# Kernel optimization log

Measured on AMD Instinct MI355X. Metric: run time of the kernel, lower is better.

Reference implementation:

```python
import jax, jax.numpy as jnp
import numpy as np

N_ENT = 50000
N_REL = 500
N_EDGE = 800000
D_IN = 100
D_OUT = 100
ALPHA = 0.2  # LeakyReLU negative slope


def setup_inputs() -> dict:
    key = jax.random.key(0)
    k0, k1, k2, k3, k4 = jax.random.split(key, 5)
    entity_embedding = jax.random.normal(k0, (N_ENT, D_IN), dtype=jnp.float32) * 0.1
    relation_embedding = jax.random.normal(k1, (N_REL, D_IN), dtype=jnp.float32) * 0.1
    W = jax.random.normal(k2, (D_IN, D_OUT), dtype=jnp.float32) * 0.1
    edge_index = jax.random.randint(k3, (2, N_EDGE), 0, N_ENT, dtype=jnp.int32)
    edge_type = jax.random.randint(k4, (N_EDGE,), 0, N_REL, dtype=jnp.int32)
    return {
        "entity_embedding": entity_embedding,
        "relation_embedding": relation_embedding,
        "W": W,
        "edge_index": edge_index,
        "edge_type": edge_type,
    }


def reference(entity_embedding, relation_embedding, W, edge_index, edge_type):
    N = entity_embedding.shape[0]
    # project input embeddings with shared W (in_features -> out_features)
    ent = entity_embedding @ W          # [N_ent, D]
    rel = relation_embedding @ W        # [N_rel, D]

    h = edge_index[0]                   # destination / head nodes [E]
    t = edge_index[1]                   # source / tail nodes      [E]

    # TransE edge score: ||h + r - t||_2 per edge
    diff = ent[h] + rel[edge_type] - ent[t]          # [E, D]
    score = jnp.sqrt(jnp.sum(diff * diff, axis=1))   # [E]
    e = jax.nn.leaky_relu(score, negative_slope=ALPHA)

    # scatter-softmax over edges grouped by head node
    seg_max = jax.ops.segment_max(e, h, num_segments=N)         # [N]
    seg_max = jnp.where(jnp.isfinite(seg_max), seg_max, 0.0)    # empty segments -> -inf
    ex = jnp.exp(e - seg_max[h])                                 # [E]
    denom = jax.ops.segment_sum(ex, h, num_segments=N)          # [N]
    att = ex / (denom[h] + 1e-16)                                # [E]

    # message: composition 'sub' of tail embedding and relation, weighted by attention
    msg = (ent[t] - rel[edge_type]) * att[:, None]               # [E, D]
    out = jax.ops.segment_sum(msg, h, num_segments=N)            # [N, D]

    # concat=True -> nonlinearity (ELU, standard GAT behavior)
    return jax.nn.elu(out)
```

## Files before the change

### kernel.cpp

```cpp
#include <hip/hip_runtime.h>
#include <math.h>

#define N_ENT  50000
#define N_REL  500
#define N_EDGE 800000
#define D      100
#define ALPHA  0.2f

#define SCAN_B 256
#define NBLK_SCAN ((N_ENT + SCAN_B - 1) / SCAN_B)

#define PROJ_TPB  256
#define PROJ_RPB  50
#define PROJ_RPT  25
#define WT_STRIDE 101

__global__ __launch_bounds__(PROJ_TPB) void proj_kernel(const float* __restrict__ X,
                                                        const float* __restrict__ W,
                                                        float* __restrict__ Y) {
    __shared__ float WT[D * WT_STRIDE];
    __shared__ float Xs[PROJ_RPB * D];
    int t = threadIdx.x;

    for (int i = t; i < D * D; i += PROJ_TPB) {
        int k = i / D, c = i % D;
        WT[c * WT_STRIDE + k] = W[i];
    }
    size_t xbase = (size_t)blockIdx.x * PROJ_RPB * D;
    for (int i = t; i < PROJ_RPB * D; i += PROJ_TPB)
        Xs[i] = X[xbase + i];
    __syncthreads();

    if (t < 200) {
        int c  = t % 100;
        int r0 = (t / 100) * PROJ_RPT;
        const float* wt = &WT[c * WT_STRIDE];
        for (int j = 0; j < PROJ_RPT; j += 5) {
            const float* x0 = &Xs[(r0 + j    ) * D];
            const float* x1 = &Xs[(r0 + j + 1) * D];
            const float* x2 = &Xs[(r0 + j + 2) * D];
            const float* x3 = &Xs[(r0 + j + 3) * D];
            const float* x4 = &Xs[(r0 + j + 4) * D];
            float a0 = 0.f, a1 = 0.f, a2 = 0.f, a3 = 0.f, a4 = 0.f;
            #pragma unroll
            for (int k = 0; k < D; ++k) {
                float w = wt[k];
                a0 = fmaf(x0[k], w, a0);
                a1 = fmaf(x1[k], w, a1);
                a2 = fmaf(x2[k], w, a2);
                a3 = fmaf(x3[k], w, a3);
                a4 = fmaf(x4[k], w, a4);
            }
            Y[xbase + (size_t)(r0 + j    ) * D + c] = a0;
            Y[xbase + (size_t)(r0 + j + 1) * D + c] = a1;
            Y[xbase + (size_t)(r0 + j + 2) * D + c] = a2;
            Y[xbase + (size_t)(r0 + j + 3) * D + c] = a3;
            Y[xbase + (size_t)(r0 + j + 4) * D + c] = a4;
        }
    }
}

__global__ void degree_kernel(const int* __restrict__ h_idx, int* __restrict__ deg) {
    int e = blockIdx.x * blockDim.x + threadIdx.x;
    if (e < N_EDGE) atomicAdd(&deg[h_idx[e]], 1);
}

__global__ void scan1_kernel(const int* __restrict__ deg, int* __restrict__ bsum) {
    __shared__ int s[SCAN_B];
    int i = blockIdx.x * SCAN_B + threadIdx.x;
    s[threadIdx.x] = (i < N_ENT) ? deg[i] : 0;
    __syncthreads();
    for (int off = SCAN_B / 2; off; off >>= 1) {
        if (threadIdx.x < off) s[threadIdx.x] += s[threadIdx.x + off];
        __syncthreads();
    }
    if (threadIdx.x == 0) bsum[blockIdx.x] = s[0];
}

__global__ void scan2_kernel(const int* __restrict__ bsum, int* __restrict__ boff) {
    __shared__ int s[SCAN_B];
    int tid = threadIdx.x;
    int v = (tid < NBLK_SCAN) ? bsum[tid] : 0;
    s[tid] = v;
    __syncthreads();
    for (int off = 1; off < SCAN_B; off <<= 1) {
        int x = (tid >= off) ? s[tid - off] : 0;
        __syncthreads();
        s[tid] += x;
        __syncthreads();
    }
    if (tid < NBLK_SCAN) boff[tid] = s[tid] - v;
}

__global__ void scan3_kernel(const int* __restrict__ deg, const int* __restrict__ boff,
                             int* __restrict__ rowptr, int* __restrict__ cursor) {
    __shared__ int s[SCAN_B];
    int tid = threadIdx.x;
    int i = blockIdx.x * SCAN_B + tid;
    int v = (i < N_ENT) ? deg[i] : 0;
    s[tid] = v;
    __syncthreads();
    for (int off = 1; off < SCAN_B; off <<= 1) {
        int x = (tid >= off) ? s[tid - off] : 0;
        __syncthreads();
        s[tid] += x;
        __syncthreads();
    }
    int excl = s[tid] - v + boff[blockIdx.x];
    if (i < N_ENT) { rowptr[i] = excl; cursor[i] = excl; }
    if (i == N_ENT - 1) rowptr[N_ENT] = excl + v;
}

__global__ void fill_kernel(const int* __restrict__ h_idx, const int* __restrict__ t_idx,
                            const int* __restrict__ etype, int* __restrict__ cursor,
                            int2* __restrict__ tr_sorted) {
    int e = blockIdx.x * blockDim.x + threadIdx.x;
    if (e >= N_EDGE) return;
    int h = h_idx[e];
    int pos = atomicAdd(&cursor[h], 1);
    tr_sorted[pos] = make_int2(t_idx[e], etype[e]);
}

__device__ __forceinline__ float edge_reduce32(const float4& eh, const float4& v) {
    float dx = eh.x + v.x, dy = eh.y + v.y, dz = eh.z + v.z, dw = eh.w + v.w;
    float s = dx * dx;
    s = fmaf(dy, dy, s);
    s = fmaf(dz, dz, s);
    s = fmaf(dw, dw, s);
    #pragma unroll
    for (int off = 16; off; off >>= 1) s += __shfl_xor(s, off, 32);
    return sqrtf(s);
}

__global__ __launch_bounds__(256) void fused_kernel(const float* __restrict__ ent,
                                                    const float* __restrict__ rel,
                                                    const int* __restrict__ rowptr,
                                                    const int2* __restrict__ tr_sorted,
                                                    float* __restrict__ out) {
    int head = blockIdx.x * 8 + (threadIdx.x >> 5);
    int lane = threadIdx.x & 31;
    if (head >= N_ENT) return;
    int beg = rowptr[head], end = rowptr[head + 1];

    float4 eh = make_float4(0.f, 0.f, 0.f, 0.f);
    if (lane < 25) eh = ((const float4*)(ent + (size_t)head * D))[lane];

    float  m   = -INFINITY;
    float  den = 0.f;
    float4 acc = make_float4(0.f, 0.f, 0.f, 0.f);

    int i = beg;
    for (; i + 1 < end; i += 2) {
        int2 e0 = tr_sorted[i];
        int2 e1 = tr_sorted[i + 1];
        float4 v0 = make_float4(0.f, 0.f, 0.f, 0.f);
        float4 v1 = make_float4(0.f, 0.f, 0.f, 0.f);
        if (lane < 25) {
            float4 et0 = ((const float4*)(ent + (size_t)e0.x * D))[lane];
            float4 er0 = ((const float4*)(rel + (size_t)e0.y * D))[lane];
            float4 et1 = ((const float4*)(ent + (size_t)e1.x * D))[lane];
            float4 er1 = ((const float4*)(rel + (size_t)e1.y * D))[lane];
            v0 = make_float4(er0.x - et0.x, er0.y - et0.y, er0.z - et0.z, er0.w - et0.w);
            v1 = make_float4(er1.x - et1.x, er1.y - et1.y, er1.z - et1.z, er1.w - et1.w);
        }
        float sc0 = edge_reduce32(eh, v0);
        float sc1 = edge_reduce32(eh, v1);

        float mn    = fmaxf(m, sc0);
        float scale = __expf(m - mn);
        float ex    = __expf(sc0 - mn);
        den   = den * scale + ex;
        acc.x = acc.x * scale - v0.x * ex;
        acc.y = acc.y * scale - v0.y * ex;
        acc.z = acc.z * scale - v0.z * ex;
        acc.w = acc.w * scale - v0.w * ex;
        m = mn;

        mn    = fmaxf(m, sc1);
        scale = __expf(m - mn);
        ex    = __expf(sc1 - mn);
        den   = den * scale + ex;
        acc.x = acc.x * scale - v1.x * ex;
        acc.y = acc.y * scale - v1.y * ex;
        acc.z = acc.z * scale - v1.z * ex;
        acc.w = acc.w * scale - v1.w * ex;
        m = mn;
    }
    if (i < end) {
        int2 e0 = tr_sorted[i];
        float4 v = make_float4(0.f, 0.f, 0.f, 0.f);
        if (lane < 25) {
            float4 et = ((const float4*)(ent + (size_t)e0.x * D))[lane];
            float4 er = ((const float4*)(rel + (size_t)e0.y * D))[lane];
            v = make_float4(er.x - et.x, er.y - et.y, er.z - et.z, er.w - et.w);
        }
        float sc = edge_reduce32(eh, v);
        float mn    = fmaxf(m, sc);
        float scale = __expf(m - mn);
        float ex    = __expf(sc - mn);
        den   = den * scale + ex;
        acc.x = acc.x * scale - v.x * ex;
        acc.y = acc.y * scale - v.y * ex;
        acc.z = acc.z * scale - v.z * ex;
        acc.w = acc.w * scale - v.w * ex;
        m = mn;
    }

    float inv = 1.f / (den + 1e-16f);
    float ox = acc.x * inv, oy = acc.y * inv, oz = acc.z * inv, ow = acc.w * inv;
    ox = ox > 0.f ? ox : expm1f(ox);
    oy = oy > 0.f ? oy : expm1f(oy);
    oz = oz > 0.f ? oz : expm1f(oz);
    ow = ow > 0.f ? ow : expm1f(ow);
    if (lane < 25)
        ((float4*)(out + (size_t)head * D))[lane] = make_float4(ox, oy, oz, ow);
}

extern "C" void kernel_launch(void* const* d_in, const int* in_sizes, int n_in,
                              void* d_out, int out_size, void* d_ws, size_t ws_size,
                              hipStream_t stream) {
    const float* entity_emb = (const float*)d_in[0];
    const float* rel_emb    = (const float*)d_in[1];
    const float* W          = (const float*)d_in[2];
    const int*   edge_index = (const int*)d_in[3];
    const int*   edge_type  = (const int*)d_in[4];
    float*       out        = (float*)d_out;

    const int* h_idx = edge_index;
    const int* t_idx = edge_index + N_EDGE;

    float* ent       = (float*)d_ws;
    float* rel       = ent + (size_t)N_ENT * D;
    int*   deg       = (int*)(rel + (size_t)N_REL * D);
    int*   rowptr    = deg + N_ENT;
    int*   cursor    = rowptr + (N_ENT + 1);
    int*   bsum      = cursor + N_ENT;
    int*   boff      = bsum + SCAN_B;
    int2*  tr_sorted = (int2*)(boff + SCAN_B);

    hipMemsetAsync(deg, 0, N_ENT * sizeof(int), stream);

    proj_kernel<<<N_ENT / PROJ_RPB, PROJ_TPB, 0, stream>>>(entity_emb, W, ent);
    proj_kernel<<<N_REL / PROJ_RPB, PROJ_TPB, 0, stream>>>(rel_emb, W, rel);

    degree_kernel<<<(N_EDGE + 255) / 256, 256, 0, stream>>>(h_idx, deg);
    scan1_kernel<<<NBLK_SCAN, SCAN_B, 0, stream>>>(deg, bsum);
    scan2_kernel<<<1, SCAN_B, 0, stream>>>(bsum, boff);
    scan3_kernel<<<NBLK_SCAN, SCAN_B, 0, stream>>>(deg, boff, rowptr, cursor);
    fill_kernel<<<(N_EDGE + 255) / 256, 256, 0, stream>>>(h_idx, t_idx, edge_type,
                                                          cursor, tr_sorted);

    fused_kernel<<<N_ENT / 8, 256, 0, stream>>>(ent, rel, rowptr, tr_sorted, out);
}
```

Baseline: 273.8 us.

## Merge projection launches, use single-block scan, unroll edge loop by four

The entity and relation projections now run in one launch, with the block index choosing the input. The three-kernel degree scan becomes a single 1024-thread block in which each thread handles 49 entries sequentially. The fused edge loop is unrolled by four so more gathers are in flight per warp. This removes three launches and their gaps and raises memory-level parallelism. The price is a serial single-block scan with strided, uncoalesced per-thread accesses, and higher register pressure in the fused kernel.

```diff
diff --git a/kernel.cpp b/kernel.cpp
--- a/kernel.cpp
+++ b/kernel.cpp
@@ -7,26 +7,33 @@
 #define D      100
 #define ALPHA  0.2f
 
-#define SCAN_B 256
-#define NBLK_SCAN ((N_ENT + SCAN_B - 1) / SCAN_B)
-
 #define PROJ_TPB  256
 #define PROJ_RPB  50
 #define PROJ_RPT  25
 #define WT_STRIDE 101
-
-__global__ __launch_bounds__(PROJ_TPB) void proj_kernel(const float* __restrict__ X,
+#define ENT_BLKS  (N_ENT / PROJ_RPB)
+#define REL_BLKS  (N_REL / PROJ_RPB)
+
+__global__ __launch_bounds__(PROJ_TPB) void proj_kernel(const float* __restrict__ Xe,
+                                                        const float* __restrict__ Xr,
                                                         const float* __restrict__ W,
-                                                        float* __restrict__ Y) {
+                                                        float* __restrict__ Ye,
+                                                        float* __restrict__ Yr) {
     __shared__ float WT[D * WT_STRIDE];
     __shared__ float Xs[PROJ_RPB * D];
     int t = threadIdx.x;
 
+    const float* X; float* Y; size_t xbase;
+    if (blockIdx.x < ENT_BLKS) {
+        X = Xe; Y = Ye; xbase = (size_t)blockIdx.x * PROJ_RPB * D;
+    } else {
+        X = Xr; Y = Yr; xbase = (size_t)(blockIdx.x - ENT_BLKS) * PROJ_RPB * D;
+    }
+
     for (int i = t; i < D * D; i += PROJ_TPB) {
         int k = i / D, c = i % D;
         WT[c * WT_STRIDE + k] = W[i];
     }
-    size_t xbase = (size_t)blockIdx.x * PROJ_RPB * D;
     for (int i = t; i < PROJ_RPB * D; i += PROJ_TPB)
         Xs[i] = X[xbase + i];
     __syncthreads();
@@ -65,50 +72,40 @@
     if (e < N_EDGE) atomicAdd(&deg[h_idx[e]], 1);
 }
 
-__global__ void scan1_kernel(const int* __restrict__ deg, int* __restrict__ bsum) {
-    __shared__ int s[SCAN_B];
-    int i = blockIdx.x * SCAN_B + threadIdx.x;
-    s[threadIdx.x] = (i < N_ENT) ? deg[i] : 0;
+#define SCAN_T   1024
+#define SCAN_EPT 49
+__global__ __launch_bounds__(SCAN_T) void scan_kernel(const int* __restrict__ deg,
+                                                      int* __restrict__ rowptr,
+                                                      int* __restrict__ cursor) {
+    __shared__ int s[SCAN_T];
+    int tid  = threadIdx.x;
+    int base = tid * SCAN_EPT;
+
+    int local = 0;
+    #pragma unroll 7
+    for (int j = 0; j < SCAN_EPT; ++j) {
+        int i = base + j;
+        if (i < N_ENT) local += deg[i];
+    }
+    s[tid] = local;
     __syncthreads();
-    for (int off = SCAN_B / 2; off; off >>= 1) {
-        if (threadIdx.x < off) s[threadIdx.x] += s[threadIdx.x + off];
-        __syncthreads();
-    }
-    if (threadIdx.x == 0) bsum[blockIdx.x] = s[0];
-}
-
-__global__ void scan2_kernel(const int* __restrict__ bsum, int* __restrict__ boff) {
-    __shared__ int s[SCAN_B];
-    int tid = threadIdx.x;
-    int v = (tid < NBLK_SCAN) ? bsum[tid] : 0;
-    s[tid] = v;
-    __syncthreads();
-    for (int off = 1; off < SCAN_B; off <<= 1) {
+    for (int off = 1; off < SCAN_T; off <<= 1) {
         int x = (tid >= off) ? s[tid - off] : 0;
         __syncthreads();
         s[tid] += x;
         __syncthreads();
     }
-    if (tid < NBLK_SCAN) boff[tid] = s[tid] - v;
-}
-
-__global__ void scan3_kernel(const int* __restrict__ deg, const int* __restrict__ boff,
-                             int* __restrict__ rowptr, int* __restrict__ cursor) {
-    __shared__ int s[SCAN_B];
-    int tid = threadIdx.x;
-    int i = blockIdx.x * SCAN_B + tid;
-    int v = (i < N_ENT) ? deg[i] : 0;
-    s[tid] = v;
-    __syncthreads();
-    for (int off = 1; off < SCAN_B; off <<= 1) {
-        int x = (tid >= off) ? s[tid - off] : 0;
-        __syncthreads();
-        s[tid] += x;
-        __syncthreads();
-    }
-    int excl = s[tid] - v + boff[blockIdx.x];
-    if (i < N_ENT) { rowptr[i] = excl; cursor[i] = excl; }
-    if (i == N_ENT - 1) rowptr[N_ENT] = excl + v;
+    int excl = s[tid] - local;
+    #pragma unroll 7
+    for (int j = 0; j < SCAN_EPT; ++j) {
+        int i = base + j;
+        if (i < N_ENT) {
+            rowptr[i] = excl;
+            cursor[i] = excl;
+            excl += deg[i];
+        }
+    }
+    if (tid == SCAN_T - 1) rowptr[N_ENT] = s[SCAN_T - 1];
 }
 
 __global__ void fill_kernel(const int* __restrict__ h_idx, const int* __restrict__ t_idx,
@@ -150,43 +147,38 @@
     float4 acc = make_float4(0.f, 0.f, 0.f, 0.f);
 
     int i = beg;
-    for (; i + 1 < end; i += 2) {
-        int2 e0 = tr_sorted[i];
-        int2 e1 = tr_sorted[i + 1];
-        float4 v0 = make_float4(0.f, 0.f, 0.f, 0.f);
-        float4 v1 = make_float4(0.f, 0.f, 0.f, 0.f);
-        if (lane < 25) {
-            float4 et0 = ((const float4*)(ent + (size_t)e0.x * D))[lane];
-            float4 er0 = ((const float4*)(rel + (size_t)e0.y * D))[lane];
-            float4 et1 = ((const float4*)(ent + (size_t)e1.x * D))[lane];
-            float4 er1 = ((const float4*)(rel + (size_t)e1.y * D))[lane];
-            v0 = make_float4(er0.x - et0.x, er0.y - et0.y, er0.z - et0.z, er0.w - et0.w);
-            v1 = make_float4(er1.x - et1.x, er1.y - et1.y, er1.z - et1.z, er1.w - et1.w);
-        }
-        float sc0 = edge_reduce32(eh, v0);
-        float sc1 = edge_reduce32(eh, v1);
-
-        float mn    = fmaxf(m, sc0);
-        float scale = __expf(m - mn);
-        float ex    = __expf(sc0 - mn);
-        den   = den * scale + ex;
-        acc.x = acc.x * scale - v0.x * ex;
-        acc.y = acc.y * scale - v0.y * ex;
-        acc.z = acc.z * scale - v0.z * ex;
-        acc.w = acc.w * scale - v0.w * ex;
-        m = mn;
-
-        mn    = fmaxf(m, sc1);
-        scale = __expf(m - mn);
-        ex    = __expf(sc1 - mn);
-        den   = den * scale + ex;
-        acc.x = acc.x * scale - v1.x * ex;
-        acc.y = acc.y * scale - v1.y * ex;
-        acc.z = acc.z * scale - v1.z * ex;
-        acc.w = acc.w * scale - v1.w * ex;
-        m = mn;
-    }
-    if (i < end) {
+    for (; i + 3 < end; i += 4) {
+        int2 ee[4];
+        float4 vv[4];
+        #pragma unroll
+        for (int u = 0; u < 4; ++u) ee[u] = tr_sorted[i + u];
+        #pragma unroll
+        for (int u = 0; u < 4; ++u) {
+            float4 v = make_float4(0.f, 0.f, 0.f, 0.f);
+            if (lane < 25) {
+                float4 et = ((const float4*)(ent + (size_t)ee[u].x * D))[lane];
+                float4 er = ((const float4*)(rel + (size_t)ee[u].y * D))[lane];
+                v = make_float4(er.x - et.x, er.y - et.y, er.z - et.z, er.w - et.w);
+            }
+            vv[u] = v;
+        }
+        float sc[4];
+        #pragma unroll
+        for (int u = 0; u < 4; ++u) sc[u] = edge_reduce32(eh, vv[u]);
+        #pragma unroll
+        for (int u = 0; u < 4; ++u) {
+            float mn    = fmaxf(m, sc[u]);
+            float scale = __expf(m - mn);
+            float ex    = __expf(sc[u] - mn);
+            den   = den * scale + ex;
+            acc.x = acc.x * scale - vv[u].x * ex;
+            acc.y = acc.y * scale - vv[u].y * ex;
+            acc.z = acc.z * scale - vv[u].z * ex;
+            acc.w = acc.w * scale - vv[u].w * ex;
+            m = mn;
+        }
+    }
+    for (; i < end; ++i) {
         int2 e0 = tr_sorted[i];
         float4 v = make_float4(0.f, 0.f, 0.f, 0.f);
         if (lane < 25) {
@@ -234,19 +226,15 @@
     int*   deg       = (int*)(rel + (size_t)N_REL * D);
     int*   rowptr    = deg + N_ENT;
     int*   cursor    = rowptr + (N_ENT + 1);
-    int*   bsum      = cursor + N_ENT;
-    int*   boff      = bsum + SCAN_B;
-    int2*  tr_sorted = (int2*)(boff + SCAN_B);
+    int2*  tr_sorted = (int2*)(cursor + N_ENT);
 
     hipMemsetAsync(deg, 0, N_ENT * sizeof(int), stream);
 
-    proj_kernel<<<N_ENT / PROJ_RPB, PROJ_TPB, 0, stream>>>(entity_emb, W, ent);
-    proj_kernel<<<N_REL / PROJ_RPB, PROJ_TPB, 0, stream>>>(rel_emb, W, rel);
+    proj_kernel<<<ENT_BLKS + REL_BLKS, PROJ_TPB, 0, stream>>>(entity_emb, rel_emb,
+                                                              W, ent, rel);
 
     degree_kernel<<<(N_EDGE + 255) / 256, 256, 0, stream>>>(h_idx, deg);
-    scan1_kernel<<<NBLK_SCAN, SCAN_B, 0, stream>>>(deg, bsum);
-    scan2_kernel<<<1, SCAN_B, 0, stream>>>(bsum, boff);
-    scan3_kernel<<<NBLK_SCAN, SCAN_B, 0, stream>>>(deg, boff, rowptr, cursor);
+    scan_kernel<<<1, SCAN_T, 0, stream>>>(deg, rowptr, cursor);
     fill_kernel<<<(N_EDGE + 255) / 256, 256, 0, stream>>>(h_idx, t_idx, edge_type,
                                                           cursor, tr_sorted);
 
```

Result: slower. 389.7 us (+42.3%).
